# Optimization experiments

Measured on AMD Instinct MI355X. Metric: run time of the kernel, lower is better.

The kernel has to match this reference:

```python
import jax, jax.numpy as jnp
import numpy as np
from jax import lax

N = 2048
D_ENC = 64      # conv channels
D = 512         # node embedding dim (resnet18 feature dim)
K = 5           # max_num_neighbors
L_LAYERS = 4    # num_layers
ARENA = 32.0    # positions scaled to [0, ARENA)^2
R2 = 2.0        # radius^2 = (sqrt(2))^2


def setup_inputs() -> dict:
    key = jax.random.key(0)
    ks = jax.random.split(key, 9)
    imgs = jax.random.normal(ks[0], (N, 3, 64, 64), dtype=jnp.float32)
    pos = jax.random.uniform(ks[1], (N, 2), dtype=jnp.float32)  # scaled by ARENA inside
    conv_w = jax.random.normal(ks[2], (D_ENC, 3, 7, 7), dtype=jnp.float32) * 0.05
    conv_b = jnp.zeros((D_ENC,), dtype=jnp.float32)
    proj_w = jax.random.normal(ks[3], (D_ENC, D), dtype=jnp.float32) * (1.0 / np.sqrt(D_ENC))
    proj_b = jnp.zeros((D,), dtype=jnp.float32)
    w_self = jax.random.normal(ks[4], (L_LAYERS, D, D), dtype=jnp.float32) * (1.0 / np.sqrt(D))
    w_nbr = jax.random.normal(ks[5], (L_LAYERS, D, D), dtype=jnp.float32) * (1.0 / np.sqrt(D))
    b_gnn = jnp.zeros((L_LAYERS, D), dtype=jnp.float32)
    return {"imgs": imgs, "pos": pos, "conv_w": conv_w, "conv_b": conv_b,
            "proj_w": proj_w, "proj_b": proj_b,
            "w_self": w_self, "w_nbr": w_nbr, "b_gnn": b_gnn}


def _encode(imgs, conv_w, conv_b, proj_w, proj_b):
    # conv 7x7 stride 2 + relu + global avg pool + linear -> [N, D]
    x = lax.conv_general_dilated(imgs, conv_w, window_strides=(2, 2), padding="SAME",
                                 dimension_numbers=("NCHW", "OIHW", "NCHW"))
    x = jax.nn.relu(x + conv_b[None, :, None, None])
    x = x.mean(axis=(2, 3))                      # [N, D_ENC]
    return jax.nn.relu(x @ proj_w + proj_b)      # [N, D]


def _radius_knn(pos):
    # radius graph with radius sqrt(2), no self loops, capped at K neighbors
    p = pos * ARENA                              # [N, 2]
    d2 = jnp.sum((p[:, None, :] - p[None, :, :]) ** 2, axis=-1)  # [N, N]
    invalid = (d2 > R2) | jnp.eye(N, dtype=bool)
    d2m = jnp.where(invalid, jnp.inf, d2)
    neg_vals, idx = lax.top_k(-d2m, K)           # K nearest within radius
    valid = jnp.isfinite(neg_vals)               # [N, K]
    return idx, valid


def reference(imgs, pos, conv_w, conv_b, proj_w, proj_b, w_self, w_nbr, b_gnn):
    h = _encode(imgs, conv_w, conv_b, proj_w, proj_b)   # [N, D]
    idx, valid = _radius_knn(pos)                        # [N, K], [N, K]
    vmask = valid.astype(h.dtype)                        # [N, K]
    denom = jnp.maximum(vmask.sum(axis=1, keepdims=True), 1.0)  # [N, 1]
    for l in range(L_LAYERS):
        nbr = h[idx] * vmask[:, :, None]                 # [N, K, D] gather
        agg = nbr.sum(axis=1) / denom                    # mean over valid neighbors
        h = jax.nn.relu(h @ w_self[l] + agg @ w_nbr[l] + b_gnn[l])
    return h
```

## Files before the change

### kernel.cpp

```cpp
#include <hip/hip_runtime.h>


#define NNODES 2048

typedef __attribute__((ext_vector_type(8))) _Float16 half8;
typedef __attribute__((ext_vector_type(16))) float f32x16;

__device__ inline uint pack2h(float x, float y) {
  ushort a = __builtin_bit_cast(ushort, (_Float16)x);
  ushort b = __builtin_bit_cast(ushort, (_Float16)y);
  return (uint)a | ((uint)b << 16);
}

__global__ __launch_bounds__(256) void setup_kernel(
    const float* __restrict__ conv_w, const float* __restrict__ wsrc_s,
    const float* __restrict__ wsrc_n, const float* __restrict__ pos,
    ushort* __restrict__ wfrag, ushort* __restrict__ wT,
    int* __restrict__ nbr, float* __restrict__ den, float* __restrict__ enc) {
  __shared__ float4 smem4[1040];
  const int bid = blockIdx.x;
  const int tid = threadIdx.x;

  if (bid < 48) {
    int i = bid * 256 + tid;
    int j = i & 7;
    int l = (i >> 3) & 63;
    int q = i >> 9;
    int kb = q % 12, ct = q / 12;
    int g = 2 * kb + (l >> 5);
    int c = 32 * ct + (l & 31);
    float val = 0.f;
    if (g < 21 && j < 7) val = conv_w[c * 147 + g * 7 + j];
    wfrag[i] = __builtin_bit_cast(ushort, (_Float16)val);
    return;
  }

  if (bid < 560) {
    float(*s)[65] = (float(*)[65])smem4;
    int bid2 = bid - 48;
    int m = bid2 >> 6, kt = (bid2 >> 3) & 7, nt = bid2 & 7;
    const float* in = (m < 4) ? (wsrc_s + m * 262144) : (wsrc_n + (m - 4) * 262144);
    ushort* out = wT + m * 262144;
    int k0 = kt << 6, n0 = nt << 6;
#pragma unroll
    for (int rep = 0; rep < 4; ++rep) {
      int row = (rep << 4) + (tid >> 4);
      int c4 = (tid & 15) << 2;
      float4 v = *(const float4*)&in[(k0 + row) * 512 + n0 + c4];
      s[row][c4] = v.x; s[row][c4 + 1] = v.y; s[row][c4 + 2] = v.z; s[row][c4 + 3] = v.w;
    }
    __syncthreads();
#pragma unroll
    for (int rep = 0; rep < 4; ++rep) {
      int n = (rep << 4) + (tid >> 4);
      int k4 = (tid & 15) << 2;
      ushort4 o;
      o.x = __builtin_bit_cast(ushort, (_Float16)s[k4 + 0][n]);
      o.y = __builtin_bit_cast(ushort, (_Float16)s[k4 + 1][n]);
      o.z = __builtin_bit_cast(ushort, (_Float16)s[k4 + 2][n]);
      o.w = __builtin_bit_cast(ushort, (_Float16)s[k4 + 3][n]);
      *(ushort4*)&out[(n0 + n) * 512 + k0 + k4] = o;
    }
    return;
  }

  {
    float* s_d2 = (float*)smem4;
    int* s_idx = (int*)(s_d2 + NNODES);
    int* s_cnt = (int*)(s_idx + NNODES);
    const int i = bid - 560;
    if (tid < 16) {
      float4 z4 = {0.f, 0.f, 0.f, 0.f};
      ((float4*)(enc + i * 64))[tid] = z4;
    }
    if (tid == 0) *s_cnt = 0;
    __syncthreads();
    const float px = pos[2 * i] * 32.f, py = pos[2 * i + 1] * 32.f;
#pragma unroll
    for (int r = 0; r < 8; ++r) {
      int j = tid + (r << 8);
      float2 q = ((const float2*)pos)[j];
      float dx = q.x * 32.f - px, dy = q.y * 32.f - py;
      float d2 = dx * dx + dy * dy;
      if (d2 <= 2.0f && j != i) {
        int slot = atomicAdd(s_cnt, 1);
        s_d2[slot] = d2;
        s_idx[slot] = j;
      }
    }
    __syncthreads();
    if (tid < 64) {
      const int lane = tid;
      const int cnt = *s_cnt;
      int nf = 0;
#pragma unroll
      for (int k = 0; k < 5; ++k) {
        float best = 1e30f;
        int bslot = 0x7fffffff;
        for (int e = lane; e < cnt; e += 64) {
          float d = s_d2[e];
          if (d < best) { best = d; bslot = e; }
        }
#pragma unroll
        for (int off = 1; off < 64; off <<= 1) {
          float od = __shfl_xor(best, off);
          int os = __shfl_xor(bslot, off);
          if (od < best || (od == best && os < bslot)) { best = od; bslot = os; }
        }
        bool got = (best < 1e30f);
        if (lane == 0) nbr[i * 5 + k] = got ? s_idx[bslot] : -1;
        if (got) { s_d2[bslot] = 1e30f; ++nf; }
      }
      if (lane == 0) den[i] = 1.f / (float)(nf > 0 ? nf : 1);
    }
  }
}

__global__ __launch_bounds__(256, 3) void conv_pool_kernel(
    const float* __restrict__ imgs, const ushort* __restrict__ wfrag,
    const float* __restrict__ cb, float* __restrict__ enc) {
  __shared__ int4 s_all[2599];
  ushort* s_img = (ushort*)s_all;
  const half8* swf8 = (const half8*)((char*)s_all + 15984);
  float* s_pool = (float*)((char*)s_all + 40560);

  const int n = blockIdx.x >> 1;
  const int r0half = blockIdx.x & 1;
  const int wy = 32 * r0half - 2;
  const int tid = threadIdx.x;
  const int lane = tid & 63;
  const int w = tid >> 6;
  const int hi = lane >> 5;
  const int lo = lane & 31;

  int4 z = {0, 0, 0, 0};
  for (int i = tid; i < 999; i += 256) s_all[i] = z;
  __syncthreads();

  const int4* wf4 = (const int4*)wfrag;
  int4* swf4 = (int4*)((char*)s_all + 15984);
#pragma unroll
  for (int r = 0; r < 6; ++r) swf4[tid + r * 256] = wf4[tid + r * 256];

  const float4* src = (const float4*)(imgs + (size_t)n * 12288);
  for (int i = tid; i < 1776; i += 256) {
    int ic = i / 592;
    int rem = i - ic * 592;
    int li = rem >> 4, xq = rem & 15;
    int iy = wy + li;
    if (iy >= 0 && iy < 64) {
      float4 v = src[(ic * 64 + iy) * 16 + xq];
      int d = (ic * 37 + li) * 72 + (xq << 2) + 2;
      ((uint*)s_img)[d >> 1] = pack2h(v.x, v.y);
      ((uint*)s_img)[(d >> 1) + 1] = pack2h(v.z, v.w);
    }
  }

  int aoff[12];
#pragma unroll
  for (int kb = 0; kb < 12; ++kb) {
    int g = 2 * kb + hi;
    if (g > 20) g = 20;
    int ic = g / 7, ky = g - ic * 7;
    aoff[kb] = (ic * 37 + ky) * 144 + 4 * lo + w * 1152;
  }
  const float bias0 = cb[lo];
  const float bias1 = cb[32 + lo];
  float pool0 = 0.f, pool1 = 0.f;
  __syncthreads();

  const char* sb = (const char*)s_img;
  union F { half8 v; uint u[4]; };

#define LOADF(F0, F1, B0, B1, KB, TPADD) do {                                 \
    const char* p_ = (const char*)__builtin_assume_aligned(                   \
        sb + aoff[KB] + (TPADD), 4);                                          \
    __builtin_memcpy(&F0.u[0], p_, 8);                                        \
    __builtin_memcpy(&F0.u[2], p_ + 8, 8);                                    \
    __builtin_memcpy(&F1.u[0], p_ + 288, 8);                                  \
    __builtin_memcpy(&F1.u[2], p_ + 296, 8);                                  \
    B0 = swf8[(KB) * 64 + lane];        B1 = swf8[(12 + (KB)) * 64 + lane];   \
  } while (0)

#pragma unroll
  for (int tp = 0; tp < 2; ++tp) {
    const int tpadd = tp * 576;
    f32x16 a0 = {}, a1 = {}, a2 = {}, a3 = {};
    F f0a, f1a, f0b, f1b;
    half8 b0a, b1a, b0b, b1b;
    LOADF(f0a, f1a, b0a, b1a, 0, tpadd);
#pragma unroll
    for (int kb = 0; kb < 12; kb += 2) {
      LOADF(f0b, f1b, b0b, b1b, kb + 1, tpadd);
      a0 = __builtin_amdgcn_mfma_f32_32x32x16_f16(f0a.v, b0a, a0, 0, 0, 0);
      a1 = __builtin_amdgcn_mfma_f32_32x32x16_f16(f0a.v, b1a, a1, 0, 0, 0);
      a2 = __builtin_amdgcn_mfma_f32_32x32x16_f16(f1a.v, b0a, a2, 0, 0, 0);
      a3 = __builtin_amdgcn_mfma_f32_32x32x16_f16(f1a.v, b1a, a3, 0, 0, 0);
      if (kb + 2 < 12) LOADF(f0a, f1a, b0a, b1a, kb + 2, tpadd);
      a0 = __builtin_amdgcn_mfma_f32_32x32x16_f16(f0b.v, b0b, a0, 0, 0, 0);
      a1 = __builtin_amdgcn_mfma_f32_32x32x16_f16(f0b.v, b1b, a1, 0, 0, 0);
      a2 = __builtin_amdgcn_mfma_f32_32x32x16_f16(f1b.v, b0b, a2, 0, 0, 0);
      a3 = __builtin_amdgcn_mfma_f32_32x32x16_f16(f1b.v, b1b, a3, 0, 0, 0);
    }
    float s0 = 0.f, s1 = 0.f;
#pragma unroll
    for (int r = 0; r < 16; ++r) {
      s0 += fmaxf(a0[r] + bias0, 0.f) + fmaxf(a2[r] + bias0, 0.f);
      s1 += fmaxf(a1[r] + bias1, 0.f) + fmaxf(a3[r] + bias1, 0.f);
    }
    pool0 += s0;
    pool1 += s1;
  }
#undef LOADF

  pool0 += __shfl_xor(pool0, 32);
  pool1 += __shfl_xor(pool1, 32);
  if (lane < 32) {
    s_pool[w * 64 + lo] = pool0;
    s_pool[w * 64 + 32 + lo] = pool1;
  }
  __syncthreads();
  if (tid < 64) {
    float s = s_pool[tid] + s_pool[64 + tid] + s_pool[128 + tid] + s_pool[192 + tid];
    atomicAdd(&enc[n * 64 + tid], s * (1.f / 1024.f));
  }
}

__global__ __launch_bounds__(256) void proj_kernel(
    const float* __restrict__ enc, const float* __restrict__ pw,
    const float* __restrict__ pb, ushort* __restrict__ h16) {
  int c = ((blockIdx.x & 1) << 8) | threadIdx.x;
  int r0 = (blockIdx.x >> 1) << 3;
  float bias = pb[c];
  float acc[8];
#pragma unroll
  for (int r = 0; r < 8; ++r) acc[r] = bias;
#pragma unroll 4
  for (int k = 0; k < 64; ++k) {
    float w = pw[k * 512 + c];
#pragma unroll
    for (int r = 0; r < 8; ++r) acc[r] = fmaf(enc[(r0 + r) * 64 + k], w, acc[r]);
  }
#pragma unroll
  for (int r = 0; r < 8; ++r)
    h16[(r0 + r) * 512 + c] = __builtin_bit_cast(ushort, (_Float16)fmaxf(acc[r], 0.f));
}

__global__ __launch_bounds__(256) void gnn_gemm_kernel(
    const ushort* __restrict__ h16, const int* __restrict__ nbr,
    const float* __restrict__ den,
    const ushort* __restrict__ Ws, const ushort* __restrict__ Wn,
    const float* __restrict__ bias, ushort* __restrict__ hout,
    float* __restrict__ fout, int final_layer) {
  __shared__ ushort s_ag[2][4096];
  __shared__ int s_nbr[320];
  __shared__ float s_den[64];
  const int tid = threadIdx.x;
  const int lane = tid & 63;
  const int hi = lane >> 5, lo = lane & 31;
  const int wu = __builtin_amdgcn_readfirstlane(tid >> 6);
  const int wr = wu >> 1, wc = wu & 1;
  const int bm = blockIdx.x >> 3, bn = blockIdx.x & 7;
  const int r0 = bm << 6, c0 = bn << 6;

  if (tid < 80) ((int4*)s_nbr)[tid] = ((const int4*)(nbr + r0 * 5))[tid];
  else if (tid < 96) ((float4*)s_den)[tid - 80] = ((const float4*)(den + r0))[tid - 80];
  __syncthreads();

  const int grow = tid >> 2, gseg = tid & 3;
  int gj[5];
  uint gm[5];
#pragma unroll
  for (int k = 0; k < 5; ++k) {
    int j = s_nbr[grow * 5 + k];
    gm[k] = (j >= 0) ? 0xFFFFFFFFu : 0u;
    gj[k] = (j >= 0) ? j : 0;
  }
  half8 den8;
  {
    _Float16 dh = (_Float16)s_den[grow];
#pragma unroll
    for (int e = 0; e < 8; ++e) den8[e] = dh;
  }

  union GU { half8 v; uint u[4]; };
  GU ga[5][2];

  auto GATHER = [&](int it) {
    const ushort* hb = h16 + (it << 6) + gseg * 16;
#pragma unroll
    for (int k = 0; k < 5; ++k) {
      const half8* p = (const half8*)(hb + gj[k] * 512);
      ga[k][0].v = p[0];
      ga[k][1].v = p[1];
    }
  };
  auto COMBINE = [&](int buf) {
#pragma unroll
    for (int part = 0; part < 2; ++part) {
      GU t0, t1, t2, t3, t4;
#pragma unroll
      for (int j2 = 0; j2 < 4; ++j2) {
        t0.u[j2] = ga[0][part].u[j2] & gm[0];
        t1.u[j2] = ga[1][part].u[j2] & gm[1];
        t2.u[j2] = ga[2][part].u[j2] & gm[2];
        t3.u[j2] = ga[3][part].u[j2] & gm[3];
        t4.u[j2] = ga[4][part].u[j2] & gm[4];
      }
      half8 s = ((t0.v + t1.v) + (t2.v + t3.v)) + t4.v;
      s = s * den8;
      *(half8*)&s_ag[buf][(2 * gseg + part) * 512 + grow * 8] = s;
    }
  };

  const ushort* pA  = h16 + (r0 + 32 * wr + lo) * 512 + 8 * hi;
  const ushort* pBs = Ws  + (c0 + 32 * wc + lo) * 512 + 8 * hi;
  const ushort* pBn = Wn  + (c0 + 32 * wc + lo) * 512 + 8 * hi;

  half8 rA[2][4], rS[2][4], rN[2][4];
#define LOADABR(P, IT) do {                                                   \
    int kk_ = (IT) << 6;                                                      \
    _Pragma("unroll")                                                         \
    for (int ks_ = 0; ks_ < 4; ++ks_) {                                       \
      rA[P][ks_] = *(const half8*)(pA  + kk_ + 16 * ks_);                     \
      rS[P][ks_] = *(const half8*)(pBs + kk_ + 16 * ks_);                     \
      rN[P][ks_] = *(const half8*)(pBn + kk_ + 16 * ks_);                     \
    }                                                                         \
  } while (0)

  f32x16 accS = {}, accN = {};
  GATHER(0);
  LOADABR(0, 0);
  COMBINE(0);
  __syncthreads();
  int cur = 0;
#pragma unroll
  for (int it = 0; it < 8; ++it) {
    const int p = it & 1;
    if (it < 7) {
      GATHER(it + 1);
      LOADABR(1 - p, it + 1);
    }
    const half8* agp = (const half8*)s_ag[cur];
#pragma unroll
    for (int ks = 0; ks < 4; ++ks) {
      accS = __builtin_amdgcn_mfma_f32_32x32x16_f16(rA[p][ks], rS[p][ks], accS, 0, 0, 0);
      half8 ag = agp[(2 * ks + hi) * 64 + 32 * wr + lo];
      accN = __builtin_amdgcn_mfma_f32_32x32x16_f16(ag, rN[p][ks], accN, 0, 0, 0);
    }
    if (it < 7) COMBINE(cur ^ 1);
    __syncthreads();
    cur ^= 1;
  }
#undef LOADABR

  const int col = c0 + 32 * wc + lo;
  const float b = bias[col];
#pragma unroll
  for (int r = 0; r < 16; ++r) {
    int row = r0 + 32 * wr + (r & 3) + ((r >> 2) << 3) + (hi << 2);
    float v = fmaxf(accS[r] + accN[r] + b, 0.f);
    if (final_layer) fout[row * 512 + col] = v;
    else hout[row * 512 + col] = __builtin_bit_cast(ushort, (_Float16)v);
  }
}

extern "C" void kernel_launch(void* const* d_in, const int* in_sizes, int n_in,
                              void* d_out, int out_size, void* d_ws, size_t ws_size,
                              hipStream_t stream) {
  const float* imgs   = (const float*)d_in[0];
  const float* pos    = (const float*)d_in[1];
  const float* conv_w = (const float*)d_in[2];
  const float* conv_b = (const float*)d_in[3];
  const float* proj_w = (const float*)d_in[4];
  const float* proj_b = (const float*)d_in[5];
  const float* w_self = (const float*)d_in[6];
  const float* w_nbr  = (const float*)d_in[7];
  const float* b_gnn  = (const float*)d_in[8];

  char* ws = (char*)d_ws;
  ushort* wfrag = (ushort*)(ws);
  float*  enc   = (float*) (ws + 32768);
  ushort* h16a  = (ushort*)(ws + 557056);
  ushort* h16b  = (ushort*)(ws + 2654208);
  ushort* wT16  = (ushort*)(ws + 6848512);
  int*    nbr   = (int*)   (ws + 11042816);
  float*  den   = (float*) (ws + 11083776);

  setup_kernel<<<2608, 256, 0, stream>>>(conv_w, w_self, w_nbr, pos,
                                         wfrag, wT16, nbr, den, enc);
  conv_pool_kernel<<<2 * NNODES, 256, 0, stream>>>(imgs, wfrag, conv_b, enc);
  proj_kernel<<<512, 256, 0, stream>>>(enc, proj_w, proj_b, h16a);

  for (int l = 0; l < 4; ++l) {
    ushort* hin  = (l & 1) ? h16b : h16a;
    ushort* hnew = (l & 1) ? h16a : h16b;
    gnn_gemm_kernel<<<256, 256, 0, stream>>>(
        hin, nbr, den, wT16 + l * 262144, wT16 + (4 + l) * 262144,
        b_gnn + l * 512, hnew, (float*)d_out, (l == 3) ? 1 : 0);
  }
}
```

Measured before the change: 151.0 us.

## Split neighbor aggregation into separate kernel and use split-K GEMM tiles

Moves the neighbor gather-and-mean out of the GEMM into a standalone agg_kernel that writes an fp16 aggregate buffer. The GEMM now uses 32x32 output tiles with the K dimension split across four waves, reduced through shared memory, and launches 1024 blocks instead of 256. This is meant to raise parallelism and occupancy and to take the irregular gather off the MFMA critical path. In exchange it adds an extra kernel launch per layer, a global round trip for the aggregate, and a shared-memory reduction.

```diff
diff --git a/kernel.cpp b/kernel.cpp
--- a/kernel.cpp
+++ b/kernel.cpp
@@ -246,120 +246,86 @@
     h16[(r0 + r) * 512 + c] = __builtin_bit_cast(ushort, (_Float16)fmaxf(acc[r], 0.f));
 }
 
+__global__ __launch_bounds__(256) void agg_kernel(
+    const ushort* __restrict__ h16, const int* __restrict__ nbr,
+    const float* __restrict__ den, ushort* __restrict__ agg16) {
+  const int gid = blockIdx.x * 256 + threadIdx.x;
+  const int i = gid >> 6;
+  const int oct = gid & 63;
+  union GU { half8 v; uint u[4]; };
+  GU t[5];
+  half8 den8;
+  {
+    _Float16 dh = (_Float16)den[i];
+#pragma unroll
+    for (int e = 0; e < 8; ++e) den8[e] = dh;
+  }
+#pragma unroll
+  for (int k = 0; k < 5; ++k) {
+    int j = nbr[i * 5 + k];
+    uint m = (j >= 0) ? 0xFFFFFFFFu : 0u;
+    const half8* p = (const half8*)(h16 + (j >= 0 ? j : 0) * 512 + oct * 8);
+    GU g;
+    g.v = *p;
+#pragma unroll
+    for (int j2 = 0; j2 < 4; ++j2) t[k].u[j2] = g.u[j2] & m;
+  }
+  half8 s = ((t[0].v + t[1].v) + (t[2].v + t[3].v)) + t[4].v;
+  s = s * den8;
+  *(half8*)&agg16[i * 512 + oct * 8] = s;
+}
+
 __global__ __launch_bounds__(256) void gnn_gemm_kernel(
-    const ushort* __restrict__ h16, const int* __restrict__ nbr,
-    const float* __restrict__ den,
+    const ushort* __restrict__ h16, const ushort* __restrict__ agg16,
     const ushort* __restrict__ Ws, const ushort* __restrict__ Wn,
     const float* __restrict__ bias, ushort* __restrict__ hout,
     float* __restrict__ fout, int final_layer) {
-  __shared__ ushort s_ag[2][4096];
-  __shared__ int s_nbr[320];
-  __shared__ float s_den[64];
+  __shared__ float s_red[4096];
   const int tid = threadIdx.x;
   const int lane = tid & 63;
   const int hi = lane >> 5, lo = lane & 31;
-  const int wu = __builtin_amdgcn_readfirstlane(tid >> 6);
-  const int wr = wu >> 1, wc = wu & 1;
-  const int bm = blockIdx.x >> 3, bn = blockIdx.x & 7;
-  const int r0 = bm << 6, c0 = bn << 6;
-
-  if (tid < 80) ((int4*)s_nbr)[tid] = ((const int4*)(nbr + r0 * 5))[tid];
-  else if (tid < 96) ((float4*)s_den)[tid - 80] = ((const float4*)(den + r0))[tid - 80];
+  const int w = tid >> 6;
+  const int bm = blockIdx.x >> 4, bn = blockIdx.x & 15;
+  const int r0 = bm << 5, c0 = bn << 5;
+
+  const ushort* pA = h16   + (r0 + lo) * 512 + (w << 7) + (hi << 3);
+  const ushort* pG = agg16 + (r0 + lo) * 512 + (w << 7) + (hi << 3);
+  const ushort* pS = Ws    + (c0 + lo) * 512 + (w << 7) + (hi << 3);
+  const ushort* pN = Wn    + (c0 + lo) * 512 + (w << 7) + (hi << 3);
+
+  f32x16 accS = {}, accN = {};
+  half8 fa[4], fg[4], fs[4], fn[4];
+#define LD(D, S) do {                                                         \
+    fa[D] = *(const half8*)(pA + 16 * (S));                                   \
+    fg[D] = *(const half8*)(pG + 16 * (S));                                   \
+    fs[D] = *(const half8*)(pS + 16 * (S));                                   \
+    fn[D] = *(const half8*)(pN + 16 * (S));                                   \
+  } while (0)
+  LD(0, 0); LD(1, 1); LD(2, 2); LD(3, 3);
+#pragma unroll
+  for (int s = 0; s < 8; ++s) {
+    const int d = s & 3;
+    accS = __builtin_amdgcn_mfma_f32_32x32x16_f16(fa[d], fs[d], accS, 0, 0, 0);
+    accN = __builtin_amdgcn_mfma_f32_32x32x16_f16(fg[d], fn[d], accN, 0, 0, 0);
+    if (s + 4 < 8) LD(d, s + 4);
+  }
+#undef LD
+
+#pragma unroll
+  for (int r = 0; r < 16; ++r)
+    s_red[(w << 10) + (r << 6) + lane] = accS[r] + accN[r];
   __syncthreads();
 
-  const int grow = tid >> 2, gseg = tid & 3;
-  int gj[5];
-  uint gm[5];
-#pragma unroll
-  for (int k = 0; k < 5; ++k) {
-    int j = s_nbr[grow * 5 + k];
-    gm[k] = (j >= 0) ? 0xFFFFFFFFu : 0u;
-    gj[k] = (j >= 0) ? j : 0;
-  }
-  half8 den8;
-  {
-    _Float16 dh = (_Float16)s_den[grow];
-#pragma unroll
-    for (int e = 0; e < 8; ++e) den8[e] = dh;
-  }
-
-  union GU { half8 v; uint u[4]; };
-  GU ga[5][2];
-
-  auto GATHER = [&](int it) {
-    const ushort* hb = h16 + (it << 6) + gseg * 16;
-#pragma unroll
-    for (int k = 0; k < 5; ++k) {
-      const half8* p = (const half8*)(hb + gj[k] * 512);
-      ga[k][0].v = p[0];
-      ga[k][1].v = p[1];
-    }
-  };
-  auto COMBINE = [&](int buf) {
-#pragma unroll
-    for (int part = 0; part < 2; ++part) {
-      GU t0, t1, t2, t3, t4;
-#pragma unroll
-      for (int j2 = 0; j2 < 4; ++j2) {
-        t0.u[j2] = ga[0][part].u[j2] & gm[0];
-        t1.u[j2] = ga[1][part].u[j2] & gm[1];
-        t2.u[j2] = ga[2][part].u[j2] & gm[2];
-        t3.u[j2] = ga[3][part].u[j2] & gm[3];
-        t4.u[j2] = ga[4][part].u[j2] & gm[4];
-      }
-      half8 s = ((t0.v + t1.v) + (t2.v + t3.v)) + t4.v;
-      s = s * den8;
-      *(half8*)&s_ag[buf][(2 * gseg + part) * 512 + grow * 8] = s;
-    }
-  };
-
-  const ushort* pA  = h16 + (r0 + 32 * wr + lo) * 512 + 8 * hi;
-  const ushort* pBs = Ws  + (c0 + 32 * wc + lo) * 512 + 8 * hi;
-  const ushort* pBn = Wn  + (c0 + 32 * wc + lo) * 512 + 8 * hi;
-
-  half8 rA[2][4], rS[2][4], rN[2][4];
-#define LOADABR(P, IT) do {                                                   \
-    int kk_ = (IT) << 6;                                                      \
-    _Pragma("unroll")                                                         \
-    for (int ks_ = 0; ks_ < 4; ++ks_) {                                       \
-      rA[P][ks_] = *(const half8*)(pA  + kk_ + 16 * ks_);                     \
-      rS[P][ks_] = *(const half8*)(pBs + kk_ + 16 * ks_);                     \
-      rN[P][ks_] = *(const half8*)(pBn + kk_ + 16 * ks_);                     \
-    }                                                                         \
-  } while (0)
-
-  f32x16 accS = {}, accN = {};
-  GATHER(0);
-  LOADABR(0, 0);
-  COMBINE(0);
-  __syncthreads();
-  int cur = 0;
-#pragma unroll
-  for (int it = 0; it < 8; ++it) {
-    const int p = it & 1;
-    if (it < 7) {
-      GATHER(it + 1);
-      LOADABR(1 - p, it + 1);
-    }
-    const half8* agp = (const half8*)s_ag[cur];
-#pragma unroll
-    for (int ks = 0; ks < 4; ++ks) {
-      accS = __builtin_amdgcn_mfma_f32_32x32x16_f16(rA[p][ks], rS[p][ks], accS, 0, 0, 0);
-      half8 ag = agp[(2 * ks + hi) * 64 + 32 * wr + lo];
-      accN = __builtin_amdgcn_mfma_f32_32x32x16_f16(ag, rN[p][ks], accN, 0, 0, 0);
-    }
-    if (it < 7) COMBINE(cur ^ 1);
-    __syncthreads();
-    cur ^= 1;
-  }
-#undef LOADABR
-
-  const int col = c0 + 32 * wc + lo;
-  const float b = bias[col];
-#pragma unroll
-  for (int r = 0; r < 16; ++r) {
-    int row = r0 + 32 * wr + (r & 3) + ((r >> 2) << 3) + (hi << 2);
-    float v = fmaxf(accS[r] + accN[r] + b, 0.f);
+  const float b = bias[c0 + lo];
+#pragma unroll
+  for (int rr = 0; rr < 4; ++rr) {
+    const int r = (w << 2) + rr;
+    const int base = (r << 6) + lane;
+    float v = s_red[base] + s_red[1024 + base] + s_red[2048 + base]
+            + s_red[3072 + base] + b;
+    v = fmaxf(v, 0.f);
+    const int row = r0 + (r & 3) + ((r >> 2) << 3) + (hi << 2);
+    const int col = c0 + lo;
     if (final_layer) fout[row * 512 + col] = v;
     else hout[row * 512 + col] = __builtin_bit_cast(ushort, (_Float16)v);
   }
@@ -383,6 +349,7 @@
   float*  enc   = (float*) (ws + 32768);
   ushort* h16a  = (ushort*)(ws + 557056);
   ushort* h16b  = (ushort*)(ws + 2654208);
+  ushort* agg16 = (ushort*)(ws + 4751360);
   ushort* wT16  = (ushort*)(ws + 6848512);
   int*    nbr   = (int*)   (ws + 11042816);
   float*  den   = (float*) (ws + 11083776);
@@ -395,8 +362,9 @@
   for (int l = 0; l < 4; ++l) {
     ushort* hin  = (l & 1) ? h16b : h16a;
     ushort* hnew = (l & 1) ? h16a : h16b;
-    gnn_gemm_kernel<<<256, 256, 0, stream>>>(
-        hin, nbr, den, wT16 + l * 262144, wT16 + (4 + l) * 262144,
+    agg_kernel<<<512, 256, 0, stream>>>(hin, nbr, den, agg16);
+    gnn_gemm_kernel<<<1024, 256, 0, stream>>>(
+        hin, agg16, wT16 + l * 262144, wT16 + (4 + l) * 262144,
         b_gnn + l * 512, hnew, (float*)d_out, (l == 3) ? 1 : 0);
   }
 }
```

Result: slower. 164.8 us (+9.1%).
